# Kernel optimization log

Measured on AMD Instinct MI355X. Metric: run time of the kernel, lower is better.

The kernel has to match this reference:

```python
import jax, jax.numpy as jnp
import numpy as np

B_SZ, SEQ, D_MODEL, D_STATE, EXPAND = 2, 1024, 1024, 16, 2
D_INNER = D_MODEL * EXPAND


def setup_inputs() -> dict:
    key = jax.random.key(0)
    ks = jax.random.split(key, 11)
    f32 = jnp.float32
    x = jax.random.normal(ks[0], (B_SZ, SEQ, D_MODEL), f32)
    # nn.Linear-style params (weight stored as [out, in], applied as x @ W.T + b)
    s_in = 1.0 / np.sqrt(D_MODEL)
    W_in = jax.random.uniform(ks[1], (2 * D_INNER, D_MODEL), f32, -s_in, s_in)
    b_in = jax.random.uniform(ks[2], (2 * D_INNER,), f32, -s_in, s_in)
    W_gate = jax.random.uniform(ks[3], (D_INNER, D_MODEL), f32, -s_in, s_in)
    b_gate = jax.random.uniform(ks[4], (D_INNER,), f32, -s_in, s_in)
    s_out = 1.0 / np.sqrt(D_INNER)
    W_out = jax.random.uniform(ks[5], (D_MODEL, D_INNER), f32, -s_out, s_out)
    b_out = jax.random.uniform(ks[6], (D_MODEL,), f32, -s_out, s_out)
    A_log = jax.random.uniform(ks[7], (D_INNER, D_STATE), f32, -3.0, -1.0)
    B_mat = 0.02 * jax.random.normal(ks[8], (D_INNER, D_STATE), f32)
    C_mat = 0.02 * jax.random.normal(ks[9], (D_INNER, D_STATE), f32)
    D_vec = 0.02 * jax.random.normal(ks[10], (D_INNER,), f32)
    return {"x": x, "W_in": W_in, "b_in": b_in, "W_gate": W_gate,
            "b_gate": b_gate, "W_out": W_out, "b_out": b_out,
            "A_log": A_log, "B_mat": B_mat, "C_mat": C_mat, "D_vec": D_vec}


def _selective_scan(x, delta, A_log, B_mat, C_mat, D_vec):
    # x, delta: [B, S, d_inner]
    A = -jnp.exp(A_log)            # [d_inner, d_state]
    c0 = C_mat[0]                  # [d_state]; torch code's [:,0,:,0] reads only C row 0

    def step(h, inp):
        x_t, d_t = inp             # each [B, d_inner]
        h = h * jnp.exp(A * d_t[..., None]) + (x_t * d_t)[..., None] * B_mat
        y_t = h @ c0               # [B, d_inner]
        return h, y_t

    h0 = jnp.zeros((x.shape[0], A.shape[0], A.shape[1]), x.dtype)
    xs = (jnp.moveaxis(x, 1, 0), jnp.moveaxis(delta, 1, 0))  # time-major
    _, ys = jax.lax.scan(step, h0, xs)                       # ys: [S, B, d_inner]
    y = jnp.moveaxis(ys, 0, 1)
    return y + x * D_vec


def reference(x, W_in, b_in, W_gate, b_gate, W_out, b_out, A_log, B_mat, C_mat, D_vec):
    gate = jax.nn.sigmoid(x @ W_gate.T + b_gate)            # [B,S,d_inner]
    proj = x @ W_in.T + b_in                                # [B,S,2*d_inner]
    x_proj, delta_proj = jnp.split(proj, 2, axis=-1)
    delta = jax.nn.relu(delta_proj)
    ss = _selective_scan(x_proj, delta, A_log, B_mat, C_mat, D_vec)
    return (gate * ss) @ W_out.T + b_out                    # [B,S,d_model]
```

## Files before the change

kernel.cpp:

```cpp
#include <hip/hip_runtime.h>
#include <hip/hip_bf16.h>


#define LOG2E 1.4426950408889634f

typedef float floatx4 __attribute__((ext_vector_type(4)));
typedef short short8 __attribute__((ext_vector_type(8)));

__device__ __forceinline__ float fexp2(float x) { return __builtin_amdgcn_exp2f(x); }
__device__ __forceinline__ unsigned short f2bf(float f) {
    unsigned int u = __float_as_uint(f);
    u = (u + 0x7fffu + ((u >> 16) & 1u)) >> 16;
    return (unsigned short)u;
}
__device__ __forceinline__ float bf2f(unsigned short h) {
    return __uint_as_float(((unsigned int)h) << 16);
}

#define GLDS16(gp, lp) __builtin_amdgcn_global_load_lds(                      \
    (const __attribute__((address_space(1))) void*)(gp),                      \
    (__attribute__((address_space(3))) void*)(lp), 16, 0, 0)

__global__ __launch_bounds__(256) void cast_and_init(
    const float* __restrict__ x, const float* __restrict__ wg,
    const float* __restrict__ wi, const float* __restrict__ wo,
    unsigned short* __restrict__ ox, unsigned short* __restrict__ owg,
    unsigned short* __restrict__ owi, unsigned short* __restrict__ owo,
    const float* __restrict__ b_out, float* __restrict__ out)
{
    const int bid = blockIdx.x;
    if (bid < 10240) {
        const size_t e = ((size_t)bid * 256 + threadIdx.x) * 4;
        const float* src; unsigned short* dst; size_t off;
        if (e < 2097152)      { src = x;  dst = ox;  off = e; }
        else if (e < 4194304) { src = wg; dst = owg; off = e - 2097152; }
        else if (e < 8388608) { src = wi; dst = owi; off = e - 4194304; }
        else                  { src = wo; dst = owo; off = e - 8388608; }
        float4 v = *(const float4*)(src + off);
        *(ushort4*)(dst + off) = make_ushort4(f2bf(v.x), f2bf(v.y), f2bf(v.z), f2bf(v.w));
    } else {
        const size_t e = ((size_t)(bid - 10240) * 256 + threadIdx.x) * 4;
        const int col = (int)(e & 1023);
        *(float4*)(out + e) = *(const float4*)(b_out + col);
    }
}

template <int MODE, int MI>
__global__ __launch_bounds__(256, 2) void gemm_mfma(
    const unsigned short* __restrict__ A,
    const unsigned short* __restrict__ W0,
    const unsigned short* __restrict__ W1,
    const float* __restrict__ bias0, const float* __restrict__ bias1,
    unsigned short* __restrict__ gate,
    float* __restrict__ xproj, float* __restrict__ delta,
    float* __restrict__ outp, int ldk, int Ksub)
{
    constexpr int BM = MI * 32;
    constexpr int ROWA = BM / 32;
    __shared__ short As[BM * 64];
    __shared__ short Bs[128 * 64];

    const int tid = threadIdx.x;
    const int l = tid & 63, w = tid >> 6;
    const int mbase = blockIdx.y * BM;
    const int kbeg = (MODE == 2) ? blockIdx.z * Ksub : 0;
    const int kend = kbeg + Ksub;

    const unsigned short* Wp; const float* bias = nullptr; int nbase; bool isGate = false;
    if (MODE == 3) {
        const int bx = blockIdx.x;
        if (bx < 16) { Wp = W0; bias = bias0; nbase = bx * 128; isGate = true; }
        else         { Wp = W1; bias = bias1; nbase = (bx - 16) * 128; }
    } else { Wp = W0; nbase = blockIdx.x * 128; }

    const int rl = l >> 3;
    const int cs = (l & 7) ^ rl;
    size_t aoff[ROWA], boff[4];
    #pragma unroll
    for (int j = 0; j < ROWA; ++j)
        aoff[j] = (size_t)(mbase + (w * ROWA + j) * 8 + rl) * ldk + cs * 8;
    #pragma unroll
    for (int j = 0; j < 4; ++j)
        boff[j] = (size_t)(nbase + (w * 4 + j) * 8 + rl) * ldk + cs * 8;

    const int wm = (w >> 1) * (MI * 16), wn = (w & 1) * 64;
    floatx4 acc[MI][4] = {};

    for (int k0 = kbeg; k0 < kend; k0 += 64) {
        __syncthreads();
        #pragma unroll
        for (int j = 0; j < ROWA; ++j)
            GLDS16(A + aoff[j] + k0, &As[(w * ROWA + j) * 512]);
        #pragma unroll
        for (int j = 0; j < 4; ++j)
            GLDS16(Wp + boff[j] + k0, &Bs[(w * 4 + j) * 512]);
        __syncthreads();

        #pragma unroll
        for (int kk = 0; kk < 2; ++kk) {
            short8 af[MI], bfr[4];
            #pragma unroll
            for (int i = 0; i < MI; ++i) {
                const int row = wm + i * 16 + (l & 15);
                af[i] = *(const short8*)&As[row * 64 + (((kk * 4 + (l >> 4)) ^ (row & 7)) << 3)];
            }
            #pragma unroll
            for (int j = 0; j < 4; ++j) {
                const int row = wn + j * 16 + (l & 15);
                bfr[j] = *(const short8*)&Bs[row * 64 + (((kk * 4 + (l >> 4)) ^ (row & 7)) << 3)];
            }
            #pragma unroll
            for (int i = 0; i < MI; ++i)
                #pragma unroll
                for (int j = 0; j < 4; ++j)
                    acc[i][j] = __builtin_amdgcn_mfma_f32_16x16x32_bf16(af[i], bfr[j], acc[i][j], 0, 0, 0);
        }
    }

    const int crow0 = wm + (l >> 4) * 4;
    const int ccol = wn + (l & 15);
    #pragma unroll
    for (int j = 0; j < 4; ++j) {
        const int n = nbase + ccol + j * 16;
        const float bb = (MODE == 2) ? 0.0f : bias[n];
        #pragma unroll
        for (int i = 0; i < MI; ++i) {
            const int mr = mbase + crow0 + i * 16;
            #pragma unroll
            for (int r = 0; r < 4; ++r) {
                const float v = acc[i][j][r] + bb;
                const int m = mr + r;
                if (MODE == 3) {
                    if (isGate) {
                        const float s = 1.0f / (1.0f + fexp2(-v * LOG2E));
                        gate[(size_t)m * 2048 + n] = f2bf(s);
                    } else if (n < 2048) {
                        xproj[(size_t)m * 2048 + n] = v;
                    } else {
                        delta[(size_t)m * 2048 + (n - 2048)] = fmaxf(v, 0.0f);
                    }
                } else {
                    atomicAdd(&outp[(size_t)m * 1024 + n], v);
                }
            }
        }
    }
}

constexpr int NC = 32, CL = 32;

__global__ __launch_bounds__(256) void scan_phaseA(
    const float* __restrict__ xp, const float* __restrict__ dl,
    const float* __restrict__ A_log, const float* __restrict__ B_mat,
    float* __restrict__ Q, float* __restrict__ sumdt)
{
    const int ch = blockIdx.x * 256 + threadIdx.x;
    const int c = blockIdx.y;
    const int d = ch & 2047, b = ch >> 11;
    float Ac[16], Bv[16], h[16];
    #pragma unroll
    for (int s = 0; s < 16; ++s) {
        Ac[s] = -fexp2(A_log[d * 16 + s] * LOG2E) * LOG2E;
        Bv[s] = B_mat[d * 16 + s];
        h[s] = 0.0f;
    }
    float sd = 0.0f;
    size_t idx = ((size_t)b * 1024 + (size_t)c * CL) * 2048 + d;
    for (int t = 0; t < CL; ++t, idx += 2048) {
        const float xt = xp[idx], dt = dl[idx];
        sd += dt;
        const float xdt = xt * dt;
        #pragma unroll
        for (int s = 0; s < 16; ++s)
            h[s] = fmaf(h[s], fexp2(Ac[s] * dt), xdt * Bv[s]);
    }
    float* q = Q + ((size_t)ch * NC + c) * 16;
    #pragma unroll
    for (int s = 0; s < 16; ++s) q[s] = h[s];
    sumdt[ch * NC + c] = sd;
}

__global__ __launch_bounds__(256) void scan_phaseB(
    const float* __restrict__ A_log, const float* __restrict__ Q,
    const float* __restrict__ sumdt, float* __restrict__ hst)
{
    const int s = threadIdx.x & 15;
    const int ch = blockIdx.x * 16 + (threadIdx.x >> 4);
    const int d = ch & 2047;
    const float Ac = -fexp2(A_log[d * 16 + s] * LOG2E) * LOG2E;
    float h = 0.0f;
    const float* q = Q + (size_t)ch * NC * 16 + s;
    const float* sd = sumdt + ch * NC;
    float* hs = hst + (size_t)ch * NC * 16 + s;
    for (int c = 0; c < NC; ++c) {
        hs[c * 16] = h;
        h = fmaf(h, fexp2(Ac * sd[c]), q[c * 16]);
    }
}

__global__ __launch_bounds__(256) void scan_phaseC(
    const float* __restrict__ xp, const float* __restrict__ dl,
    const float* __restrict__ A_log, const float* __restrict__ B_mat,
    const float* __restrict__ C_mat, const float* __restrict__ D_vec,
    const unsigned short* __restrict__ gate, const float* __restrict__ hst,
    unsigned short* __restrict__ z)
{
    const int ch = blockIdx.x * 256 + threadIdx.x;
    const int c = blockIdx.y;
    const int d = ch & 2047, b = ch >> 11;
    float Ac[16], Bv[16], Cv[16], h[16];
    #pragma unroll
    for (int s = 0; s < 16; ++s) {
        Ac[s] = -fexp2(A_log[d * 16 + s] * LOG2E) * LOG2E;
        Bv[s] = B_mat[d * 16 + s];
        Cv[s] = C_mat[s];
        h[s] = hst[((size_t)ch * NC + c) * 16 + s];
    }
    const float Dv = D_vec[d];
    size_t idx = ((size_t)b * 1024 + (size_t)c * CL) * 2048 + d;
    for (int t = 0; t < CL; ++t, idx += 2048) {
        const float xt = xp[idx], dt = dl[idx];
        const float xdt = xt * dt;
        float y = 0.0f;
        #pragma unroll
        for (int s = 0; s < 16; ++s) {
            h[s] = fmaf(h[s], fexp2(Ac[s] * dt), xdt * Bv[s]);
            y = fmaf(h[s], Cv[s], y);
        }
        const float g = bf2f(gate[idx]);
        z[idx] = f2bf(g * (y + xt * Dv));
    }
}

extern "C" void kernel_launch(void* const* d_in, const int* in_sizes, int n_in,
                              void* d_out, int out_size, void* d_ws, size_t ws_size,
                              hipStream_t stream) {
    const float* x      = (const float*)d_in[0];
    const float* W_in   = (const float*)d_in[1];
    const float* b_in   = (const float*)d_in[2];
    const float* W_gate = (const float*)d_in[3];
    const float* b_gate = (const float*)d_in[4];
    const float* W_out  = (const float*)d_in[5];
    const float* b_out  = (const float*)d_in[6];
    const float* A_log  = (const float*)d_in[7];
    const float* B_mat  = (const float*)d_in[8];
    const float* C_mat  = (const float*)d_in[9];
    const float* D_vec  = (const float*)d_in[10];
    float* out = (float*)d_out;

    float* fws = (float*)d_ws;
    float* xproj = fws;
    float* delta = xproj + 4194304;
    float* Q     = delta + 4194304;
    float* hst   = Q + 2097152;
    float* sumdt = hst + 2097152;
    unsigned short* us = (unsigned short*)(sumdt + 131072);
    unsigned short* gate  = us;
    unsigned short* z     = gate  + 4194304;
    unsigned short* x_bf  = z     + 4194304;
    unsigned short* wg_bf = x_bf  + 2097152;
    unsigned short* wi_bf = wg_bf + 2097152;
    unsigned short* wo_bf = wi_bf + 4194304;

    dim3 blk(256);
    cast_and_init<<<12288, blk, 0, stream>>>(x, W_gate, W_in, W_out,
                                             x_bf, wg_bf, wi_bf, wo_bf, b_out, out);
    gemm_mfma<3, 8><<<dim3(48, 8), blk, 0, stream>>>(
        x_bf, wg_bf, wi_bf, b_gate, b_in, gate, xproj, delta, nullptr, 1024, 1024);
    scan_phaseA<<<dim3(16, NC), blk, 0, stream>>>(xproj, delta, A_log, B_mat, Q, sumdt);
    scan_phaseB<<<256, blk, 0, stream>>>(A_log, Q, sumdt, hst);
    scan_phaseC<<<dim3(16, NC), blk, 0, stream>>>(xproj, delta, A_log, B_mat, C_mat, D_vec, gate, hst, z);
    gemm_mfma<2, 2><<<dim3(8, 32, 2), blk, 0, stream>>>(
        z, wo_bf, nullptr, nullptr, nullptr, nullptr, nullptr, nullptr, out, 2048, 1024);
}
```

Measured before the change: 212.9 us.

## Store xproj/delta as bf16 with LDS-staged vectorized epilogue and smaller GEMM tiles

The input-projection GEMM now writes xproj and delta as bf16 instead of fp32, which halves the intermediate traffic that the two scan phases re-read. Its epilogue stages the output tile in shared memory and writes coalesced 16-byte rows instead of scattered scalar stores. The tile M is also reduced from 256 to 128 (grid doubled) and the launch bound raised to 3 blocks per CU for more occupancy. The cost is lower precision in delta and xproj feeding the exponential scan, which risks accuracy drift.

```diff
diff --git a/kernel.cpp b/kernel.cpp
--- a/kernel.cpp
+++ b/kernel.cpp
@@ -46,19 +46,21 @@
 }
 
 template <int MODE, int MI>
-__global__ __launch_bounds__(256, 2) void gemm_mfma(
+__global__ __launch_bounds__(256, 3) void gemm_mfma(
     const unsigned short* __restrict__ A,
     const unsigned short* __restrict__ W0,
     const unsigned short* __restrict__ W1,
     const float* __restrict__ bias0, const float* __restrict__ bias1,
     unsigned short* __restrict__ gate,
-    float* __restrict__ xproj, float* __restrict__ delta,
+    unsigned short* __restrict__ xproj, unsigned short* __restrict__ delta,
     float* __restrict__ outp, int ldk, int Ksub)
 {
     constexpr int BM = MI * 32;
     constexpr int ROWA = BM / 32;
-    __shared__ short As[BM * 64];
-    __shared__ short Bs[128 * 64];
+    constexpr int NSH = (MODE == 3) ? 16384 : (BM * 64 + 8192);
+    __shared__ short smem[NSH];
+    short* Asd = smem;
+    short* Bsd = smem + BM * 64;
 
     const int tid = threadIdx.x;
     const int l = tid & 63, w = tid >> 6;
@@ -90,10 +92,10 @@
         __syncthreads();
         #pragma unroll
         for (int j = 0; j < ROWA; ++j)
-            GLDS16(A + aoff[j] + k0, &As[(w * ROWA + j) * 512]);
+            GLDS16(A + aoff[j] + k0, &Asd[(w * ROWA + j) * 512]);
         #pragma unroll
         for (int j = 0; j < 4; ++j)
-            GLDS16(Wp + boff[j] + k0, &Bs[(w * 4 + j) * 512]);
+            GLDS16(Wp + boff[j] + k0, &Bsd[(w * 4 + j) * 512]);
         __syncthreads();
 
         #pragma unroll
@@ -102,12 +104,12 @@
             #pragma unroll
             for (int i = 0; i < MI; ++i) {
                 const int row = wm + i * 16 + (l & 15);
-                af[i] = *(const short8*)&As[row * 64 + (((kk * 4 + (l >> 4)) ^ (row & 7)) << 3)];
+                af[i] = *(const short8*)&Asd[row * 64 + (((kk * 4 + (l >> 4)) ^ (row & 7)) << 3)];
             }
             #pragma unroll
             for (int j = 0; j < 4; ++j) {
                 const int row = wn + j * 16 + (l & 15);
-                bfr[j] = *(const short8*)&Bs[row * 64 + (((kk * 4 + (l >> 4)) ^ (row & 7)) << 3)];
+                bfr[j] = *(const short8*)&Bsd[row * 64 + (((kk * 4 + (l >> 4)) ^ (row & 7)) << 3)];
             }
             #pragma unroll
             for (int i = 0; i < MI; ++i)
@@ -117,40 +119,54 @@
         }
     }
 
-    const int crow0 = wm + (l >> 4) * 4;
-    const int ccol = wn + (l & 15);
-    #pragma unroll
-    for (int j = 0; j < 4; ++j) {
-        const int n = nbase + ccol + j * 16;
-        const float bb = (MODE == 2) ? 0.0f : bias[n];
-        #pragma unroll
-        for (int i = 0; i < MI; ++i) {
-            const int mr = mbase + crow0 + i * 16;
-            #pragma unroll
-            for (int r = 0; r < 4; ++r) {
-                const float v = acc[i][j][r] + bb;
-                const int m = mr + r;
-                if (MODE == 3) {
-                    if (isGate) {
-                        const float s = 1.0f / (1.0f + fexp2(-v * LOG2E));
-                        gate[(size_t)m * 2048 + n] = f2bf(s);
-                    } else if (n < 2048) {
-                        xproj[(size_t)m * 2048 + n] = v;
-                    } else {
-                        delta[(size_t)m * 2048 + (n - 2048)] = fmaxf(v, 0.0f);
-                    }
-                } else {
-                    atomicAdd(&outp[(size_t)m * 1024 + n], v);
+    const int mt = wm + (l >> 4) * 4;
+    const int nt = wn + (l & 15);
+    if (MODE == 3) {
+        __syncthreads();
+        unsigned short* lout = (unsigned short*)smem;
+        #pragma unroll
+        for (int j = 0; j < 4; ++j) {
+            const float bb = bias[nbase + nt + j * 16];
+            #pragma unroll
+            for (int i = 0; i < MI; ++i) {
+                #pragma unroll
+                for (int r = 0; r < 4; ++r) {
+                    float v = acc[i][j][r] + bb;
+                    if (isGate) v = 1.0f / (1.0f + fexp2(-v * LOG2E));
+                    else if (nbase >= 2048) v = fmaxf(v, 0.0f);
+                    lout[(mt + i * 16 + r) * 128 + nt + j * 16] = f2bf(v);
                 }
             }
         }
+        __syncthreads();
+        unsigned short* dst = isGate ? gate : (nbase < 2048 ? xproj : delta);
+        const int ncb = nbase & 2047;
+        #pragma unroll
+        for (int it = 0; it < 8; ++it) {
+            const int so = it * 2048 + tid * 8;
+            const int mrow = so >> 7, ncol = so & 127;
+            short8 v = *(const short8*)&lout[so];
+            *(short8*)&dst[(size_t)(mbase + mrow) * 2048 + ncb + ncol] = v;
+        }
+    } else {
+        #pragma unroll
+        for (int j = 0; j < 4; ++j) {
+            const int n = nbase + nt + j * 16;
+            #pragma unroll
+            for (int i = 0; i < MI; ++i) {
+                #pragma unroll
+                for (int r = 0; r < 4; ++r)
+                    atomicAdd(&outp[(size_t)(mbase + mt + i * 16 + r) * 1024 + n],
+                              acc[i][j][r]);
+            }
+        }
     }
 }
 
 constexpr int NC = 32, CL = 32;
 
 __global__ __launch_bounds__(256) void scan_phaseA(
-    const float* __restrict__ xp, const float* __restrict__ dl,
+    const unsigned short* __restrict__ xp, const unsigned short* __restrict__ dl,
     const float* __restrict__ A_log, const float* __restrict__ B_mat,
     float* __restrict__ Q, float* __restrict__ sumdt)
 {
@@ -167,7 +183,7 @@
     float sd = 0.0f;
     size_t idx = ((size_t)b * 1024 + (size_t)c * CL) * 2048 + d;
     for (int t = 0; t < CL; ++t, idx += 2048) {
-        const float xt = xp[idx], dt = dl[idx];
+        const float xt = bf2f(xp[idx]), dt = bf2f(dl[idx]);
         sd += dt;
         const float xdt = xt * dt;
         #pragma unroll
@@ -199,7 +215,7 @@
 }
 
 __global__ __launch_bounds__(256) void scan_phaseC(
-    const float* __restrict__ xp, const float* __restrict__ dl,
+    const unsigned short* __restrict__ xp, const unsigned short* __restrict__ dl,
     const float* __restrict__ A_log, const float* __restrict__ B_mat,
     const float* __restrict__ C_mat, const float* __restrict__ D_vec,
     const unsigned short* __restrict__ gate, const float* __restrict__ hst,
@@ -219,7 +235,7 @@
     const float Dv = D_vec[d];
     size_t idx = ((size_t)b * 1024 + (size_t)c * CL) * 2048 + d;
     for (int t = 0; t < CL; ++t, idx += 2048) {
-        const float xt = xp[idx], dt = dl[idx];
+        const float xt = bf2f(xp[idx]), dt = bf2f(dl[idx]);
         const float xdt = xt * dt;
         float y = 0.0f;
         #pragma unroll
@@ -249,15 +265,15 @@
     float* out = (float*)d_out;
 
     float* fws = (float*)d_ws;
-    float* xproj = fws;
-    float* delta = xproj + 4194304;
-    float* Q     = delta + 4194304;
+    float* Q     = fws;
     float* hst   = Q + 2097152;
     float* sumdt = hst + 2097152;
     unsigned short* us = (unsigned short*)(sumdt + 131072);
     unsigned short* gate  = us;
     unsigned short* z     = gate  + 4194304;
-    unsigned short* x_bf  = z     + 4194304;
+    unsigned short* xproj = z     + 4194304;
+    unsigned short* delta = xproj + 4194304;
+    unsigned short* x_bf  = delta + 4194304;
     unsigned short* wg_bf = x_bf  + 2097152;
     unsigned short* wi_bf = wg_bf + 2097152;
     unsigned short* wo_bf = wi_bf + 4194304;
@@ -265,7 +281,7 @@
     dim3 blk(256);
     cast_and_init<<<12288, blk, 0, stream>>>(x, W_gate, W_in, W_out,
                                              x_bf, wg_bf, wi_bf, wo_bf, b_out, out);
-    gemm_mfma<3, 8><<<dim3(48, 8), blk, 0, stream>>>(
+    gemm_mfma<3, 4><<<dim3(48, 16), blk, 0, stream>>>(
         x_bf, wg_bf, wi_bf, b_gate, b_in, gate, xproj, delta, nullptr, 1024, 1024);
     scan_phaseA<<<dim3(16, NC), blk, 0, stream>>>(xproj, delta, A_log, B_mat, Q, sumdt);
     scan_phaseB<<<256, blk, 0, stream>>>(A_log, Q, sumdt, hst);
```

Measured after the change: 208.5 us. 2.1% less time.
